# Kernel optimization log

Measured on AMD Instinct MI355X. Metric: run time of the kernel, lower is better.

## Reference

```python
import jax, jax.numpy as jnp
import numpy as np

NEG_BIG = -9e15  # matches -9000000000000000.0 in the torch source
ALPHA = 0.2      # LeakyReLU negative slope


def setup_inputs() -> dict:
    key = jax.random.key(0)
    k1, k2, k3, k4 = jax.random.split(key, 4)
    N, F_in, F_out = 8192, 256, 128
    x = jax.random.normal(k1, (N, F_in), dtype=jnp.float32)
    adj = jax.random.randint(k2, (N, N), 0, 2, dtype=jnp.int32)
    W = jax.random.normal(k3, (F_in, F_out), dtype=jnp.float32) * 0.05
    a = jax.random.normal(k4, (2 * F_out, 1), dtype=jnp.float32) * 0.05
    return {"x": x, "adj": adj, "W": W, "a": a}


def reference(x, adj, W, a):
    # h = x @ W : [N, F]
    h = x @ W
    F_out = W.shape[1]
    # Algebraically identical to the concat formulation:
    # a^T [h_i || h_j] = h_i @ a1 + h_j @ a2
    a1 = a[:F_out, 0]
    a2 = a[F_out:, 0]
    src = h @ a1  # [N]
    dst = h @ a2  # [N]
    e = jax.nn.leaky_relu(src[:, None] + dst[None, :], negative_slope=ALPHA)  # [N, N]
    attention = jnp.where(adj > 0, e, NEG_BIG)
    attention = jax.nn.softmax(attention, axis=1)
    # dropout is identity in eval mode (training=False)
    h_prime = attention @ h  # [N, F]
    return h_prime
```

## Files before the change

kernel.cpp:

```cpp
#include <hip/hip_runtime.h>
#include <cstdint>

#define N 8192
#define FIN 256
#define FOUT 128
#define ALPHA 0.2f
#define JP 2
#define JSL (N / JP)
#define TJ 64
#define NTILE (JSL / TJ)
#define RB 32
#define SST 72

typedef unsigned short u16;
typedef unsigned char u8;
typedef __attribute__((ext_vector_type(8))) short short8;
typedef __attribute__((ext_vector_type(4))) float floatx4;

__device__ __forceinline__ u16 bf16_rne(float f) {
  uint32_t u = __float_as_uint(f);
  u += 0x7fff + ((u >> 16) & 1);
  return (u16)(u >> 16);
}

__device__ __forceinline__ void gl_lds16(const void* g, void* l) {
  __builtin_amdgcn_global_load_lds(
      (const __attribute__((address_space(1))) void*)g,
      (__attribute__((address_space(3))) void*)l, 16, 0, 0);
}

__global__ __launch_bounds__(256) void k_proj(const float* __restrict__ x,
                                              const float* __restrict__ W,
                                              const float* __restrict__ a,
                                              u16* __restrict__ hT3,
                                              float* __restrict__ srcv,
                                              float* __restrict__ dstv) {
  __shared__ float xs[8 * FIN];
  __shared__ float partS[4][4], partD[4][4];
  const int t = threadIdx.x;
  const int R0 = blockIdx.x * 8;

  const float4* xv = (const float4*)(x + (size_t)R0 * FIN);
  float4* xsv = (float4*)xs;
  xsv[t] = xv[t];
  xsv[t + 256] = xv[t + 256];
  __syncthreads();

  const int c  = t & 127;
  const int rg = (t >> 7) * 4;

  float acc[4] = {0.f, 0.f, 0.f, 0.f};
  float wa[4], wb[4];
  #pragma unroll
  for (int j = 0; j < 4; ++j) wa[j] = W[j * FOUT + c];
  #pragma unroll
  for (int j = 0; j < 4; ++j) wb[j] = W[(4 + j) * FOUT + c];

  for (int k4 = 0; k4 < FIN / 4; ++k4) {
    float wc[4];
    #pragma unroll
    for (int j = 0; j < 4; ++j) { wc[j] = wa[j]; wa[j] = wb[j]; }
    const int kn = (k4 + 2 < FIN / 4) ? k4 + 2 : k4;
    #pragma unroll
    for (int j = 0; j < 4; ++j) wb[j] = W[(kn * 4 + j) * FOUT + c];
    #pragma unroll
    for (int i = 0; i < 4; ++i) {
      const float4 xq = *(const float4*)&xs[(rg + i) * FIN + k4 * 4];
      acc[i] += xq.x * wc[0] + xq.y * wc[1] + xq.z * wc[2] + xq.w * wc[3];
    }
  }

  {
    const int j = R0 + rg;
    const int jb = j >> 5, q = (j >> 3) & 3, jj = j & 7;
    const int m = c & 15, nt = c >> 4;
    union { u16 u[4]; uint2 v; } pk;
    #pragma unroll
    for (int i = 0; i < 4; ++i) pk.u[i] = bf16_rne(acc[i]);
    *(uint2*)(hT3 + (size_t)(((jb * 8 + nt) * 64) + (m * 4 + q)) * 8 + jj) = pk.v;
  }

  const float a1 = a[c], a2 = a[FOUT + c];
  float s4[4], d4[4];
  #pragma unroll
  for (int i = 0; i < 4; ++i) { s4[i] = acc[i] * a1; d4[i] = acc[i] * a2; }
  #pragma unroll
  for (int off = 32; off > 0; off >>= 1) {
    #pragma unroll
    for (int i = 0; i < 4; ++i) {
      s4[i] += __shfl_down(s4[i], off);
      d4[i] += __shfl_down(d4[i], off);
    }
  }
  const int wv = t >> 6, lane = t & 63;
  if (lane == 0) {
    #pragma unroll
    for (int i = 0; i < 4; ++i) { partS[wv][i] = s4[i]; partD[wv][i] = d4[i]; }
  }
  __syncthreads();
  if (t < 16) {
    const int i = t & 3, rg2 = (t >> 2) & 1, which = t >> 3;
    if (which == 0) srcv[R0 + rg2 * 4 + i] = partS[rg2*2][i] + partS[rg2*2+1][i];
    else            dstv[R0 + rg2 * 4 + i] = partD[rg2*2][i] + partD[rg2*2+1][i];
  }
}

__global__ __launch_bounds__(256, 2) void k_gat(const int* __restrict__ adj,
                                                const u16* __restrict__ hT3,
                                                const float* __restrict__ srcv,
                                                const float* __restrict__ dstv,
                                                float* __restrict__ P,
                                                float* __restrict__ lp) {
  __shared__ u16 hS[2][8192];
  __shared__ int adjS[2][2048];
  __shared__ u16 S[RB * SST];
  const int t = threadIdx.x;
  const int wv = t >> 6, lane = t & 63;
  const int q = lane >> 4, m = lane & 15;
  const int bm = blockIdx.x & 255;
  const int jp = blockIdx.x >> 8;
  const int R0 = bm * RB;
  const int j0 = jp * JSL;

  const int pr = t >> 3;
  const int pc = (t & 7) * 8;
  const float srcr = srcv[R0 + pr];
  const float* dstp = dstv + j0 + pc;

  const int rh = wv & 1, ch = wv >> 1;
  const int Lq = m * 4 + q;

  floatx4 acc[4];
  #pragma unroll
  for (int nt = 0; nt < 4; ++nt) acc[nt] = (floatx4){0.f, 0.f, 0.f, 0.f};
  float lsum = 0.f;

  const size_t jb00 = (size_t)(j0 >> 5);
  #define STAGE(I, BUF)                                                        \
  {                                                                            \
    _Pragma("unroll")                                                          \
    for (int cc = 0; cc < 4; ++cc) {                                           \
      const int kc = wv * 4 + cc;                                   \
      const int jbl = kc >> 3, nt_ = kc & 7;                                   \
      const u16* src = hT3 + ((jb00 + (size_t)(I) * 2 + jbl) * 8 + nt_) * 512  \
                       + (size_t)lane * 8;                                     \
      gl_lds16(src, &hS[BUF][kc * 512]);                                       \
    }                                                                          \
    _Pragma("unroll")                                                          \
    for (int cc = 0; cc < 2; ++cc) {                                           \
      const int c_ = wv * 2 + cc;                                    \
      const int* asrc = adj + (size_t)(R0 + c_ * 4 + (lane >> 4)) * N          \
                        + j0 + (I) * TJ + (lane & 15) * 4;                     \
      gl_lds16(asrc, &adjS[BUF][c_ * 256]);                                    \
    }                                                                          \
  }

  STAGE(0, 0)
  __builtin_amdgcn_sched_barrier(0);
  float4 dC0 = *(const float4*)(dstp),   dC1 = *(const float4*)(dstp + 4);

  int buf = 0;
  for (int i = 0; i < NTILE; ++i) {
    asm volatile("s_waitcnt vmcnt(2) lgkmcnt(0)" ::: "memory");
    __builtin_amdgcn_s_barrier();
    __builtin_amdgcn_sched_barrier(0);

    const int4 A0 = *((const int4*)adjS[buf] + pr * 16 + (t & 7) * 2);
    const int4 A1 = *((const int4*)adjS[buf] + pr * 16 + (t & 7) * 2 + 1);

    const int nx = (i + 1 < NTILE) ? i + 1 : i;
    if (i + 1 < NTILE) STAGE(i + 1, buf ^ 1)
    __builtin_amdgcn_sched_barrier(0);
    float4 dN0 = *(const float4*)(dstp + nx * TJ);
    float4 dN1 = *(const float4*)(dstp + nx * TJ + 4);

    {
      const int   ai[8] = {A0.x, A0.y, A0.z, A0.w, A1.x, A1.y, A1.z, A1.w};
      const float df[8] = {dC0.x, dC0.y, dC0.z, dC0.w, dC1.x, dC1.y, dC1.z, dC1.w};
      union { u16 u[8]; short8 s; } pk;
      #pragma unroll
      for (int e = 0; e < 8; ++e) {
        float v = srcr + df[e];
        v = fmaxf(v, ALPHA * v);
        const float p = ai[e] > 0 ? __expf(v) : 0.f;
        lsum += p;
        pk.u[e] = bf16_rne(p);
      }
      *(short8*)&S[pr * SST + pc] = pk.s;
    }

    asm volatile("s_waitcnt lgkmcnt(0)" ::: "memory");
    __builtin_amdgcn_s_barrier();
    __builtin_amdgcn_sched_barrier(0);

    {
      const short8 a0 = *(const short8*)&S[(rh * 16 + m) * SST + q * 8];
      const short8 a1 = *(const short8*)&S[(rh * 16 + m) * SST + 32 + q * 8];
      #pragma unroll
      for (int nt = 0; nt < 4; ++nt) {
        const short8 b0 = *(const short8*)&hS[buf][(0 * 8 + ch * 4 + nt) * 512 + Lq * 8];
        const short8 b1 = *(const short8*)&hS[buf][(1 * 8 + ch * 4 + nt) * 512 + Lq * 8];
        acc[nt] = __builtin_amdgcn_mfma_f32_16x16x32_bf16(a0, b0, acc[nt], 0, 0, 0);
        acc[nt] = __builtin_amdgcn_mfma_f32_16x16x32_bf16(a1, b1, acc[nt], 0, 0, 0);
      }
    }

    dC0 = dN0; dC1 = dN1;
    buf ^= 1;
  }
  #undef STAGE

  lsum += __shfl_down(lsum, 4);
  lsum += __shfl_down(lsum, 2);
  lsum += __shfl_down(lsum, 1);
  if ((t & 7) == 0) lp[(size_t)jp * N + R0 + pr] = lsum;

  float* Pp = P + ((size_t)jp * N + R0 + rh * 16) * FOUT + ch * 64;
  #pragma unroll
  for (int nt = 0; nt < 4; ++nt)
    #pragma unroll
    for (int ri = 0; ri < 4; ++ri)
      Pp[(size_t)(q * 4 + ri) * FOUT + nt * 16 + m] = acc[nt][ri];
}

__global__ __launch_bounds__(256) void k_norm(const float* __restrict__ P,
                                              const float* __restrict__ lp,
                                              float* __restrict__ out) {
  const int idx = blockIdx.x * 256 + threadIdx.x;
  const int rr = idx >> 5;
  const int c4 = (idx & 31) * 4;
  float l = 0.f;
  #pragma unroll
  for (int j = 0; j < JP; ++j) l += lp[j * N + rr];
  const float inv = 1.0f / l;
  float4 s = {0.f, 0.f, 0.f, 0.f};
  #pragma unroll
  for (int j = 0; j < JP; ++j) {
    const float4 p = *(const float4*)(P + ((size_t)j * N + rr) * FOUT + c4);
    s.x += p.x; s.y += p.y; s.z += p.z; s.w += p.w;
  }
  s.x *= inv; s.y *= inv; s.z *= inv; s.w *= inv;
  *(float4*)(out + (size_t)rr * FOUT + c4) = s;
}

extern "C" void kernel_launch(void* const* d_in, const int* in_sizes, int n_in,
                              void* d_out, int out_size, void* d_ws, size_t ws_size,
                              hipStream_t stream) {
  const float* x   = (const float*)d_in[0];
  const int*   adj = (const int*)d_in[1];
  const float* W   = (const float*)d_in[2];
  const float* a   = (const float*)d_in[3];
  float* out = (float*)d_out;

  char* ws = (char*)d_ws;
  u16*   hT3  = (u16*)ws;     ws += (size_t)FOUT * N * sizeof(u16);
  float* srcv = (float*)ws;   ws += (size_t)N * sizeof(float);
  float* dstv = (float*)ws;   ws += (size_t)N * sizeof(float);
  float* P    = (float*)ws;   ws += (size_t)JP * N * FOUT * sizeof(float);
  float* lp   = (float*)ws;   ws += (size_t)JP * N * sizeof(float);

  k_proj<<<N / 8, 256, 0, stream>>>(x, W, a, hT3, srcv, dstv);
  k_gat <<<256 * JP, 256, 0, stream>>>(adj, hT3, srcv, dstv, P, lp);
  k_norm<<<(N * FOUT / 4) / 256, 256, 0, stream>>>(P, lp, out);
}
```

Before: 429.5 us.

## Triple-buffer h and adj tiles to prefetch two tiles ahead

Moves the LDS staging of h and adj tiles from double to triple buffering, so each iteration issues async global-to-LDS loads for tile i+2 while computing tile i. Buffers rotate by pointer, the wait becomes vmcnt(8), and the last tile is peeled into an epilogue. The aim is to hide more global-load latency behind the exp/pack and MFMA phases. The cost is about 77KB of LDS per block instead of about 53KB, which can lower the number of resident blocks per CU.

New measurement: 430.5 us. Within noise of the previous version (+0.2%).

```diff
diff --git a/kernel.cpp b/kernel.cpp
--- a/kernel.cpp
+++ b/kernel.cpp
@@ -111,8 +111,8 @@
                                                 const float* __restrict__ dstv,
                                                 float* __restrict__ P,
                                                 float* __restrict__ lp) {
-  __shared__ u16 hS[2][8192];
-  __shared__ int adjS[2][2048];
+  __shared__ u16 hS[3][8192];
+  __shared__ int adjS[3][2048];
   __shared__ u16 S[RB * SST];
   const int t = threadIdx.x;
   const int wv = t >> 6, lane = t & 63;
@@ -135,8 +135,11 @@
   for (int nt = 0; nt < 4; ++nt) acc[nt] = (floatx4){0.f, 0.f, 0.f, 0.f};
   float lsum = 0.f;
 
+  u16* h0 = &hS[0][0]; u16* h1 = &hS[1][0]; u16* h2 = &hS[2][0];
+  int* a0 = &adjS[0][0]; int* a1 = &adjS[1][0]; int* a2 = &adjS[2][0];
+
   const size_t jb00 = (size_t)(j0 >> 5);
-  #define STAGE(I, BUF)                                                        \
+  #define STAGE(I, HD, AD)                                                     \
   {                                                                            \
     _Pragma("unroll")                                                          \
     for (int cc = 0; cc < 4; ++cc) {                                           \
@@ -144,71 +147,96 @@
       const int jbl = kc >> 3, nt_ = kc & 7;                                   \
       const u16* src = hT3 + ((jb00 + (size_t)(I) * 2 + jbl) * 8 + nt_) * 512  \
                        + (size_t)lane * 8;                                     \
-      gl_lds16(src, &hS[BUF][kc * 512]);                                       \
+      gl_lds16(src, (HD) + kc * 512);                                          \
     }                                                                          \
     _Pragma("unroll")                                                          \
     for (int cc = 0; cc < 2; ++cc) {                                           \
       const int c_ = wv * 2 + cc;                                    \
       const int* asrc = adj + (size_t)(R0 + c_ * 4 + (lane >> 4)) * N          \
                         + j0 + (I) * TJ + (lane & 15) * 4;                     \
-      gl_lds16(asrc, &adjS[BUF][c_ * 256]);                                    \
-    }                                                                          \
-  }
-
-  STAGE(0, 0)
+      gl_lds16(asrc, (AD) + c_ * 256);                                         \
+    }                                                                          \
+  }
+
+  #define PPHASE(A0_, A1_, dC0_, dC1_)                                         \
+  {                                                                            \
+    const int   ai[8] = {A0_.x, A0_.y, A0_.z, A0_.w, A1_.x, A1_.y, A1_.z, A1_.w}; \
+    const float df[8] = {dC0_.x, dC0_.y, dC0_.z, dC0_.w, dC1_.x, dC1_.y, dC1_.z, dC1_.w}; \
+    union { u16 u[8]; short8 s; } pk;                                          \
+    _Pragma("unroll")                                                          \
+    for (int e = 0; e < 8; ++e) {                                              \
+      float v = srcr + df[e];                                                  \
+      v = fmaxf(v, ALPHA * v);                                                 \
+      const float p = ai[e] > 0 ? __expf(v) : 0.f;                             \
+      lsum += p;                                                               \
+      pk.u[e] = bf16_rne(p);                                                   \
+    }                                                                          \
+    *(short8*)&S[pr * SST + pc] = pk.s;                                        \
+  }
+
+  #define MFMAPH(HB)                                                           \
+  {                                                                            \
+    const short8 a0f = *(const short8*)&S[(rh * 16 + m) * SST + q * 8];        \
+    const short8 a1f = *(const short8*)&S[(rh * 16 + m) * SST + 32 + q * 8];   \
+    _Pragma("unroll")                                                          \
+    for (int nt = 0; nt < 4; ++nt) {                                           \
+      const short8 b0 = *(const short8*)&(HB)[(0 * 8 + ch * 4 + nt) * 512 + Lq * 8]; \
+      const short8 b1 = *(const short8*)&(HB)[(1 * 8 + ch * 4 + nt) * 512 + Lq * 8]; \
+      acc[nt] = __builtin_amdgcn_mfma_f32_16x16x32_bf16(a0f, b0, acc[nt], 0, 0, 0); \
+      acc[nt] = __builtin_amdgcn_mfma_f32_16x16x32_bf16(a1f, b1, acc[nt], 0, 0, 0); \
+    }                                                                          \
+  }
+
+  STAGE(0, h0, a0)
   __builtin_amdgcn_sched_barrier(0);
   float4 dC0 = *(const float4*)(dstp),   dC1 = *(const float4*)(dstp + 4);
-
-  int buf = 0;
-  for (int i = 0; i < NTILE; ++i) {
-    asm volatile("s_waitcnt vmcnt(2) lgkmcnt(0)" ::: "memory");
+  __builtin_amdgcn_sched_barrier(0);
+  STAGE(1, h1, a1)
+  __builtin_amdgcn_sched_barrier(0);
+
+  for (int i = 0; i < NTILE - 1; ++i) {
+    asm volatile("s_waitcnt vmcnt(8) lgkmcnt(0)" ::: "memory");
     __builtin_amdgcn_s_barrier();
     __builtin_amdgcn_sched_barrier(0);
 
-    const int4 A0 = *((const int4*)adjS[buf] + pr * 16 + (t & 7) * 2);
-    const int4 A1 = *((const int4*)adjS[buf] + pr * 16 + (t & 7) * 2 + 1);
-
-    const int nx = (i + 1 < NTILE) ? i + 1 : i;
-    if (i + 1 < NTILE) STAGE(i + 1, buf ^ 1)
-    __builtin_amdgcn_sched_barrier(0);
-    float4 dN0 = *(const float4*)(dstp + nx * TJ);
-    float4 dN1 = *(const float4*)(dstp + nx * TJ + 4);
-
-    {
-      const int   ai[8] = {A0.x, A0.y, A0.z, A0.w, A1.x, A1.y, A1.z, A1.w};
-      const float df[8] = {dC0.x, dC0.y, dC0.z, dC0.w, dC1.x, dC1.y, dC1.z, dC1.w};
-      union { u16 u[8]; short8 s; } pk;
-      #pragma unroll
-      for (int e = 0; e < 8; ++e) {
-        float v = srcr + df[e];
-        v = fmaxf(v, ALPHA * v);
-        const float p = ai[e] > 0 ? __expf(v) : 0.f;
-        lsum += p;
-        pk.u[e] = bf16_rne(p);
-      }
-      *(short8*)&S[pr * SST + pc] = pk.s;
-    }
+    const int4 A0 = *((const int4*)a0 + pr * 16 + (t & 7) * 2);
+    const int4 A1 = *((const int4*)a0 + pr * 16 + (t & 7) * 2 + 1);
+    __builtin_amdgcn_sched_barrier(0);
+
+    float4 dN0 = *(const float4*)(dstp + (i + 1) * TJ);
+    float4 dN1 = *(const float4*)(dstp + (i + 1) * TJ + 4);
+    __builtin_amdgcn_sched_barrier(0);
+    if (i + 2 < NTILE) STAGE(i + 2, h2, a2)
+    __builtin_amdgcn_sched_barrier(0);
+
+    PPHASE(A0, A1, dC0, dC1)
 
     asm volatile("s_waitcnt lgkmcnt(0)" ::: "memory");
     __builtin_amdgcn_s_barrier();
     __builtin_amdgcn_sched_barrier(0);
 
-    {
-      const short8 a0 = *(const short8*)&S[(rh * 16 + m) * SST + q * 8];
-      const short8 a1 = *(const short8*)&S[(rh * 16 + m) * SST + 32 + q * 8];
-      #pragma unroll
-      for (int nt = 0; nt < 4; ++nt) {
-        const short8 b0 = *(const short8*)&hS[buf][(0 * 8 + ch * 4 + nt) * 512 + Lq * 8];
-        const short8 b1 = *(const short8*)&hS[buf][(1 * 8 + ch * 4 + nt) * 512 + Lq * 8];
-        acc[nt] = __builtin_amdgcn_mfma_f32_16x16x32_bf16(a0, b0, acc[nt], 0, 0, 0);
-        acc[nt] = __builtin_amdgcn_mfma_f32_16x16x32_bf16(a1, b1, acc[nt], 0, 0, 0);
-      }
-    }
-
+    MFMAPH(h0)
+
+    u16* ht = h0; h0 = h1; h1 = h2; h2 = ht;
+    int* at = a0; a0 = a1; a1 = a2; a2 = at;
     dC0 = dN0; dC1 = dN1;
-    buf ^= 1;
-  }
+  }
+
+  asm volatile("s_waitcnt vmcnt(2) lgkmcnt(0)" ::: "memory");
+  __builtin_amdgcn_s_barrier();
+  __builtin_amdgcn_sched_barrier(0);
+  {
+    const int4 A0 = *((const int4*)a0 + pr * 16 + (t & 7) * 2);
+    const int4 A1 = *((const int4*)a0 + pr * 16 + (t & 7) * 2 + 1);
+    PPHASE(A0, A1, dC0, dC1)
+  }
+  asm volatile("s_waitcnt lgkmcnt(0)" ::: "memory");
+  __builtin_amdgcn_s_barrier();
+  __builtin_amdgcn_sched_barrier(0);
+  MFMAPH(h0)
   #undef STAGE
+  #undef PPHASE
+  #undef MFMAPH
 
   lsum += __shfl_down(lsum, 4);
   lsum += __shfl_down(lsum, 2);
```
